# Performance work log

Measured on AMD Instinct MI355X. Metric: run time of the kernel, lower is better.

## Reference

```python
import jax, jax.numpy as jnp
import numpy as np

D_MODEL = 2048
NUM_HEADS = 16
NUM_KV_HEADS = 4
LATENT_DIM = 64
HEAD_DIM = D_MODEL // NUM_HEADS  # 128
GROUP_SIZE = NUM_HEADS // NUM_KV_HEADS  # 4
B, T = 4, 2048


def setup_inputs() -> dict:
    key = jax.random.key(0)
    ks = jax.random.split(key, 9)
    s = lambda fan_in: 1.0 / np.sqrt(fan_in)
    # weights stored as (in, out) so y = x @ W matches torch Linear math
    return {
        "x": jax.random.normal(ks[0], (B, T, D_MODEL), jnp.float32),
        "W_q": jax.random.uniform(ks[1], (D_MODEL, D_MODEL), jnp.float32, -s(D_MODEL), s(D_MODEL)),
        "W_k": jax.random.uniform(ks[2], (D_MODEL, NUM_KV_HEADS * HEAD_DIM), jnp.float32, -s(D_MODEL), s(D_MODEL)),
        "W_v": jax.random.uniform(ks[3], (D_MODEL, NUM_KV_HEADS * HEAD_DIM), jnp.float32, -s(D_MODEL), s(D_MODEL)),
        "W_k_to_latent": jax.random.uniform(ks[4], (HEAD_DIM, LATENT_DIM), jnp.float32, -s(HEAD_DIM), s(HEAD_DIM)),
        "W_v_to_latent": jax.random.uniform(ks[5], (HEAD_DIM, LATENT_DIM), jnp.float32, -s(HEAD_DIM), s(HEAD_DIM)),
        "W_k_from_latent": jax.random.uniform(ks[6], (LATENT_DIM, HEAD_DIM), jnp.float32, -s(LATENT_DIM), s(LATENT_DIM)),
        "W_v_from_latent": jax.random.uniform(ks[7], (LATENT_DIM, HEAD_DIM), jnp.float32, -s(LATENT_DIM), s(LATENT_DIM)),
        "W_o": jax.random.uniform(ks[8], (D_MODEL, D_MODEL), jnp.float32, -s(D_MODEL), s(D_MODEL)),
    }


def reference(x, W_q, W_k, W_v, W_k_to_latent, W_v_to_latent, W_k_from_latent, W_v_from_latent, W_o):
    b, t, _ = x.shape
    # projections
    q = (x @ W_q).reshape(b, t, NUM_HEADS, HEAD_DIM).transpose(0, 2, 1, 3)        # [B,H,T,Dh]
    k = (x @ W_k).reshape(b, t, NUM_KV_HEADS, HEAD_DIM).transpose(0, 2, 1, 3)     # [B,Hkv,T,Dh]
    v = (x @ W_v).reshape(b, t, NUM_KV_HEADS, HEAD_DIM).transpose(0, 2, 1, 3)
    # compress to latent, then restore (explicit, as in the original module)
    k_latent = k @ W_k_to_latent                                                  # [B,Hkv,T,L]
    v_latent = v @ W_v_to_latent
    k_restored = k_latent @ W_k_from_latent                                       # [B,Hkv,T,Dh]
    v_restored = v_latent @ W_v_from_latent
    # GQA tiling: repeat_interleave over head axis
    k_tile = jnp.repeat(k_restored, GROUP_SIZE, axis=1)                           # [B,H,T,Dh]
    v_tile = jnp.repeat(v_restored, GROUP_SIZE, axis=1)
    # explicit attention
    att = jnp.einsum("bhqd,bhkd->bhqk", q, k_tile) / jnp.sqrt(jnp.float32(HEAD_DIM))
    p = jax.nn.softmax(att, axis=-1)
    ctx = jnp.einsum("bhqk,bhkd->bhqd", p, v_tile)                                # [B,H,T,Dh]
    ctx = ctx.transpose(0, 2, 1, 3).reshape(b, t, D_MODEL)
    return ctx @ W_o
```

## Files before the change

### kernel.cpp

```cpp
#include <hip/hip_runtime.h>

typedef __attribute__((ext_vector_type(8))) short short8;
typedef __attribute__((ext_vector_type(4))) float f32x4;
typedef __attribute__((ext_vector_type(16))) float f32x16;
typedef __attribute__((ext_vector_type(4))) unsigned short us4;
typedef __attribute__((ext_vector_type(4))) int i32x4;
typedef __bf16 bf16x2v __attribute__((ext_vector_type(2)));

__device__ __forceinline__ unsigned short f2bf(float f) {
  unsigned u = __builtin_bit_cast(unsigned, f);
  u += 0x7FFFu + ((u >> 16) & 1u);
  return (unsigned short)(u >> 16);
}

__device__ __forceinline__ int packbf(float lo, float hi) {
  bf16x2v v = {(__bf16)lo, (__bf16)hi};
  return __builtin_bit_cast(int, v);
}

__device__ __forceinline__ void gll16(const void* g, void* l) {
  __builtin_amdgcn_global_load_lds(
      (const __attribute__((address_space(1))) void*)g,
      (__attribute__((address_space(3))) void*)l, 16, 0, 0);
}

__device__ __forceinline__ f32x4 MFMA(short8 a, short8 b, f32x4 c) {
  return __builtin_amdgcn_mfma_f32_16x16x32_bf16(a, b, c, 0, 0, 0);
}
__device__ __forceinline__ f32x16 MFMA32(short8 a, short8 b, f32x16 c) {
  return __builtin_amdgcn_mfma_f32_32x32x16_bf16(a, b, c, 0, 0, 0);
}


__global__ void conv_bf16(const float* __restrict__ in, unsigned short* __restrict__ out, int n4) {
  for (int i = blockIdx.x * blockDim.x + threadIdx.x; i < n4; i += gridDim.x * blockDim.x) {
    float4 v = ((const float4*)in)[i];
    us4 o;
    o[0] = f2bf(v.x); o[1] = f2bf(v.y); o[2] = f2bf(v.z); o[3] = f2bf(v.w);
    ((us4*)out)[i] = o;
  }
}

__global__ void t32x2(const float* __restrict__ a, const float* __restrict__ b,
                      float* __restrict__ oa, float* __restrict__ ob) {
  __shared__ float tile[32][33];
  const float* in = blockIdx.z ? b : a;
  float* out = blockIdx.z ? ob : oa;
  int bx = blockIdx.x, by = blockIdx.y;
  int tx = threadIdx.x, ty = threadIdx.y;
#pragma unroll
  for (int i = 0; i < 4; ++i)
    tile[ty + i * 8][tx] = in[(long)(by * 32 + ty + i * 8) * 128 + bx * 32 + tx];
  __syncthreads();
#pragma unroll
  for (int i = 0; i < 4; ++i)
    out[(long)(bx * 32 + ty + i * 8) * 64 + by * 32 + tx] = tile[tx][ty + i * 8];
}

__global__ void fold_q(const float* __restrict__ Wq, const float* __restrict__ WkflT,
                       float* __restrict__ out, float sc) {
  const int t = threadIdx.x;
  const int l = t & 63, wv = t >> 6;
  const int k = blockIdx.x;
  const float* wq = Wq + (long)k * 2048 + wv * 4 * 128;
  float acc[4] = {};
  for (int d = 0; d < 128; ++d) {
    float fv = WkflT[d * 64 + l];
#pragma unroll
    for (int i = 0; i < 4; ++i) acc[i] += wq[i * 128 + d] * fv;
  }
  float* orow = out + (long)k * 1024 + wv * 4 * 64;
#pragma unroll
  for (int i = 0; i < 4; ++i) orow[i * 64 + l] = acc[i] * sc;
}

__global__ void fold_kv2(const float* __restrict__ Wk, const float* __restrict__ Wv,
                         const float* __restrict__ Wk2l, const float* __restrict__ Wv2l,
                         float* __restrict__ out) {
  const int z = blockIdx.z;
  const float* W = z ? Wv : Wk;
  const float* W2l = z ? Wv2l : Wk2l;
  int l = threadIdx.x;
  int k = blockIdx.x;
  int hk = blockIdx.y;
  const float* wr = W + (long)k * 512 + hk * 128;
  float acc = 0.f;
#pragma unroll 8
  for (int d = 0; d < 128; ++d) acc += wr[d] * W2l[d * 64 + l];
  out[(long)k * 512 + z * 256 + hk * 64 + l] = acc;
}

__global__ void tconv2(const float* __restrict__ a, unsigned short* __restrict__ oq,
                       const float* __restrict__ b, unsigned short* __restrict__ okv) {
  __shared__ float tile[32][33];
  int bx = blockIdx.x, by = blockIdx.y;
  int tx = threadIdx.x, ty = threadIdx.y;
  const float* in;
  unsigned short* out;
  int C;
  if (bx < 32) { in = a; out = oq; C = 1024; }
  else         { in = b; out = okv; C = 512; bx -= 32; }
#pragma unroll
  for (int i = 0; i < 4; ++i)
    tile[ty + i * 8][tx] = in[(long)(by * 32 + ty + i * 8) * C + bx * 32 + tx];
  __syncthreads();
#pragma unroll
  for (int i = 0; i < 4; ++i)
    out[(long)(bx * 32 + ty + i * 8) * 2048 + by * 32 + tx] = f2bf(tile[tx][ty + i * 8]);
}

__global__ void fold_o(const float* __restrict__ WvflT, const float* __restrict__ Wo,
                       unsigned short* __restrict__ WoLatT) {
  const int l = threadIdx.x;
  const int j0 = blockIdx.x * 16;
  const int h = blockIdx.y;
  const float* wo = Wo + (long)h * 128 * 2048 + j0;
  float acc[16] = {};
  for (int d = 0; d < 128; ++d) {
    float fv = WvflT[d * 64 + l];
    const float* wr = wo + (long)d * 2048;
#pragma unroll
    for (int jj = 0; jj < 16; ++jj) acc[jj] += fv * wr[jj];
  }
#pragma unroll
  for (int jj = 0; jj < 16; ++jj)
    WoLatT[(long)(j0 + jj) * 1024 + h * 64 + l] = f2bf(acc[jj]);
}

template <int EPI>
__global__ __launch_bounds__(256, 2) void gemm_bt(const unsigned short* __restrict__ A,
                                                  const unsigned short* __restrict__ BT,
                                                  void* __restrict__ Cout, int M, int N, int K) {
  __shared__ unsigned short As[128 * 32];
  __shared__ unsigned short Bs[128 * 32];
  const int tid = threadIdx.x;
  const int lane = tid & 63, w = tid >> 6;
  const int wr = w >> 1, wc = w & 1;
  const int c = lane & 15, hi = lane >> 4;
  const int nbn = N >> 7;
  int bid = blockIdx.x;
  bid = (bid & 7) * (gridDim.x >> 3) + (bid >> 3);
  const int bm = bid / nbn, bn = bid % nbn;
  const int row0 = bm << 7, col0 = bn << 7;

  const unsigned short* ga = A + (long)(row0 + (tid >> 2)) * K + ((tid & 3) << 3);
  const unsigned short* gb = BT + (long)(col0 + (tid >> 2)) * K + ((tid & 3) << 3);
  unsigned short* la = As + tid * 8;
  unsigned short* lb = Bs + tid * 8;
  const long sA = (long)64 * K;

  f32x4 acc[4][4] = {};

  for (int k0 = 0; k0 < K; k0 += 32) {
    __syncthreads();
    gll16(ga + k0, la);
    gll16(ga + sA + k0, la + 2048);
    gll16(gb + k0, lb);
    gll16(gb + sA + k0, lb + 2048);
    __syncthreads();
    short8 a[4], b[4];
#pragma unroll
    for (int m = 0; m < 4; ++m)
      a[m] = *(const short8*)&As[(wr * 64 + m * 16 + c) * 32 + hi * 8];
#pragma unroll
    for (int n = 0; n < 4; ++n)
      b[n] = *(const short8*)&Bs[(wc * 64 + n * 16 + c) * 32 + hi * 8];
#pragma unroll
    for (int m = 0; m < 4; ++m)
#pragma unroll
      for (int n = 0; n < 4; ++n) acc[m][n] = MFMA(a[m], b[n], acc[m][n]);
  }

  if (EPI == 0) {
    unsigned short* C = (unsigned short*)Cout;
#pragma unroll
    for (int m = 0; m < 4; ++m) {
      int r0 = row0 + wr * 64 + m * 16 + hi * 4;
#pragma unroll
      for (int n = 0; n < 4; ++n) {
        int cc = col0 + wc * 64 + n * 16 + c;
#pragma unroll
        for (int j = 0; j < 4; ++j) C[(long)(r0 + j) * N + cc] = f2bf(acc[m][n][j]);
      }
    }
  } else {
    float* C = (float*)Cout;
#pragma unroll
    for (int m = 0; m < 4; ++m) {
      int r0 = row0 + wr * 64 + m * 16 + hi * 4;
#pragma unroll
      for (int n = 0; n < 4; ++n) {
        int cc = col0 + wc * 64 + n * 16 + c;
#pragma unroll
        for (int j = 0; j < 4; ++j) C[(long)(r0 + j) * N + cc] = acc[m][n][j];
      }
    }
  }
}

__global__ __launch_bounds__(256, 2) void gemm_qkv(const unsigned short* __restrict__ A,
                                                   const unsigned short* __restrict__ BT,
                                                   unsigned short* __restrict__ Qout,
                                                   unsigned short* __restrict__ Kout,
                                                   unsigned short* __restrict__ Vout) {
  const int K = 2048;
  __shared__ unsigned short As[128 * 32];
  __shared__ unsigned short Bs[128 * 32];
  const int tid = threadIdx.x;
  const int lane = tid & 63, w = tid >> 6;
  const int wr = w >> 1, wc = w & 1;
  const int c = lane & 15, hi = lane >> 4;
  const int nbn = 12;
  int bid = blockIdx.x;
  bid = (bid & 7) * (gridDim.x >> 3) + (bid >> 3);
  const int bm = bid / nbn, bn = bid % nbn;
  const int row0 = bm << 7, col0 = bn << 7;

  const unsigned short* ga = A + (long)(row0 + (tid >> 2)) * K + ((tid & 3) << 3);
  const unsigned short* gb = BT + (long)(col0 + (tid >> 2)) * K + ((tid & 3) << 3);
  unsigned short* la = As + tid * 8;
  unsigned short* lb = Bs + tid * 8;
  const long sA = (long)64 * K;

  f32x4 acc[4][4] = {};

  for (int k0 = 0; k0 < K; k0 += 32) {
    __syncthreads();
    gll16(ga + k0, la);
    gll16(ga + sA + k0, la + 2048);
    gll16(gb + k0, lb);
    gll16(gb + sA + k0, lb + 2048);
    __syncthreads();
    short8 a[4], b[4];
#pragma unroll
    for (int m = 0; m < 4; ++m)
      a[m] = *(const short8*)&As[(wr * 64 + m * 16 + c) * 32 + hi * 8];
#pragma unroll
    for (int n = 0; n < 4; ++n)
      b[n] = *(const short8*)&Bs[(wc * 64 + n * 16 + c) * 32 + hi * 8];
#pragma unroll
    for (int m = 0; m < 4; ++m)
#pragma unroll
      for (int n = 0; n < 4; ++n) acc[m][n] = MFMA(a[m], b[n], acc[m][n]);
  }

  if (col0 < 1024) {
#pragma unroll
    for (int m = 0; m < 4; ++m) {
      int r0 = row0 + wr * 64 + m * 16 + hi * 4;
#pragma unroll
      for (int n = 0; n < 4; ++n) {
        int cc = col0 + wc * 64 + n * 16 + c;
#pragma unroll
        for (int j = 0; j < 4; ++j) Qout[(long)(r0 + j) * 1024 + cc] = f2bf(acc[m][n][j]);
      }
    }
  } else if (col0 < 1280) {
#pragma unroll
    for (int m = 0; m < 4; ++m) {
      int r0 = row0 + wr * 64 + m * 16 + hi * 4;
#pragma unroll
      for (int n = 0; n < 4; ++n) {
        int cc = col0 - 1024 + wc * 64 + n * 16 + c;
#pragma unroll
        for (int j = 0; j < 4; ++j) Kout[(long)(r0 + j) * 256 + cc] = f2bf(acc[m][n][j]);
      }
    }
  } else {
#pragma unroll
    for (int m = 0; m < 4; ++m) {
      int r0 = row0 + wr * 64 + m * 16 + hi * 4;
#pragma unroll
      for (int n = 0; n < 4; ++n) {
        int cc = col0 - 1280 + wc * 64 + n * 16 + c;
        us4 v;
#pragma unroll
        for (int j = 0; j < 4; ++j) v[j] = f2bf(acc[m][n][j]);
        *(us4*)&Vout[(long)cc * 8192 + r0] = v;
      }
    }
  }
}

__global__ __launch_bounds__(512, 1) void attn_kernel(const unsigned short* __restrict__ Q,
                                                      const unsigned short* __restrict__ Kr,
                                                      const unsigned short* __restrict__ VT,
                                                      unsigned short* __restrict__ CTX) {
  const int qt = blockIdx.x, h = blockIdx.y, b = blockIdx.z;
  const int kvh = h >> 2;
  const int tid = threadIdx.x, lane = tid & 63, w = tid >> 6;
  const int q31 = lane & 31, hi = lane >> 5;

  __shared__ unsigned short Ks[2][64 * 64];
  __shared__ unsigned short Vs[2][64 * 64];

  const long qrow = (long)(b * 2048 + qt * 256 + w * 32 + q31);
  short8 qf[4];
#pragma unroll
  for (int st = 0; st < 4; ++st)
    qf[st] = *(const short8*)&Q[qrow * 1024 + h * 64 + st * 16 + hi * 8];

  f32x16 acc[2] = {};
  f32x16 acc_s = {};
  short8 ones;
#pragma unroll
  for (int e = 0; e < 8; ++e) ones[e] = (short)0x3F80;

  const unsigned short* kbase = Kr + (long)b * 2048 * 256 + kvh * 64;
  const unsigned short* vbase = VT + (long)kvh * 64 * 8192 + b * 2048;

  const int p = tid * 16;
  const int srow = p >> 8;
  const int inb = (p & 255) ^ ((srow & 15) << 4);
  const int skey = srow * 2 + (inb >> 7);
  const long kgo = (long)skey * 256 + ((inb & 127) >> 1);
  const long vgo = (long)skey * 8192 + ((inb & 127) >> 1);

#define STAGE(T, BUF)                                     \
  do {                                                    \
    gll16(kbase + (long)(T) * 16384 + kgo, (char*)Ks[BUF] + p); \
    gll16(vbase + (T) * 64 + vgo, (char*)Vs[BUF] + p);    \
  } while (0)

  STAGE(0, 0);
  __syncthreads();

  const int kr0 = q31 >> 1, kr1 = 16 + (q31 >> 1);
  const int ki0 = (q31 & 1) * 128;
  const int kswz0 = (kr0 & 15) << 4;
  const int kswz1 = (kr1 & 15) << 4;

  for (int t = 0; t < 32; ++t) {
    const int cur = t & 1;
    if (t < 31) STAGE(t + 1, cur ^ 1);

    const char* ks = (const char*)Ks[cur];
    const char* vs = (const char*)Vs[cur];

    f32x16 s0 = {}, s1 = {};
    __builtin_amdgcn_s_setprio(1);
#pragma unroll
    for (int st = 0; st < 4; ++st) {
      int colb = st * 32 + hi * 16;
      short8 k0 = *(const short8*)(ks + kr0 * 256 + ((ki0 + colb) ^ kswz0));
      short8 k1 = *(const short8*)(ks + kr1 * 256 + ((ki0 + colb) ^ kswz1));
      s0 = MFMA32(k0, qf[st], s0);
      s1 = MFMA32(k1, qf[st], s1);
    }
    __builtin_amdgcn_s_setprio(0);

#pragma unroll
    for (int e = 0; e < 16; ++e) s0[e] = __builtin_amdgcn_exp2f(s0[e]);
#pragma unroll
    for (int e = 0; e < 16; ++e) s1[e] = __builtin_amdgcn_exp2f(s1[e]);

    short8 ap[4];
#pragma unroll
    for (int kq = 0; kq < 4; ++kq) {
      int a0, a1, a2, a3;
      if (kq == 0) {
        a0 = packbf(s0[0], s0[1]);   a1 = packbf(s0[2], s0[3]);
        a2 = packbf(s0[4], s0[5]);   a3 = packbf(s0[6], s0[7]);
      } else if (kq == 1) {
        a0 = packbf(s0[8], s0[9]);   a1 = packbf(s0[10], s0[11]);
        a2 = packbf(s0[12], s0[13]); a3 = packbf(s0[14], s0[15]);
      } else if (kq == 2) {
        a0 = packbf(s1[0], s1[1]);   a1 = packbf(s1[2], s1[3]);
        a2 = packbf(s1[4], s1[5]);   a3 = packbf(s1[6], s1[7]);
      } else {
        a0 = packbf(s1[8], s1[9]);   a1 = packbf(s1[10], s1[11]);
        a2 = packbf(s1[12], s1[13]); a3 = packbf(s1[14], s1[15]);
      }
      int off0 = hi ? a0 : a2;
      int off1 = hi ? a1 : a3;
      int r0 = __shfl_xor(off0, 32);
      int r1 = __shfl_xor(off1, 32);
      i32x4 tt;
      tt[0] = hi ? r0 : a0;
      tt[1] = hi ? r1 : a1;
      tt[2] = hi ? a2 : r0;
      tt[3] = hi ? a3 : r1;
      ap[kq] = __builtin_bit_cast(short8, tt);
    }

    __builtin_amdgcn_s_setprio(1);
#pragma unroll
    for (int dblk = 0; dblk < 2; ++dblk) {
      int d = dblk * 32 + q31;
      int vr = d >> 1;
      int vi = (d & 1) * 128;
      int vswz = (vr & 15) << 4;
#pragma unroll
      for (int kq = 0; kq < 4; ++kq) {
        short8 vv = *(const short8*)(vs + vr * 256 + ((vi + kq * 32 + hi * 16) ^ vswz));
        acc[dblk] = MFMA32(ap[kq], vv, acc[dblk]);
      }
    }
#pragma unroll
    for (int kq = 0; kq < 4; ++kq) acc_s = MFMA32(ap[kq], ones, acc_s);
    __builtin_amdgcn_s_setprio(0);

    __syncthreads();
  }

#pragma unroll
  for (int rg = 0; rg < 16; ++rg) {
    int qr = (rg & 3) + 8 * (rg >> 2) + 4 * hi;
    float il = 1.0f / acc_s[rg];
    long grow = (long)(b * 2048 + qt * 256 + w * 32 + qr);
#pragma unroll
    for (int dblk = 0; dblk < 2; ++dblk)
      CTX[grow * 1024 + h * 64 + dblk * 32 + q31] = f2bf(acc[dblk][rg] * il);
  }
#undef STAGE
}


extern "C" void kernel_launch(void* const* d_in, const int* in_sizes, int n_in, void* d_out,
                              int out_size, void* d_ws, size_t ws_size, hipStream_t stream) {
  (void)in_sizes; (void)n_in; (void)out_size; (void)ws_size;
  const float* x    = (const float*)d_in[0];
  const float* W_q  = (const float*)d_in[1];
  const float* W_k  = (const float*)d_in[2];
  const float* W_v  = (const float*)d_in[3];
  const float* Wk2l = (const float*)d_in[4];
  const float* Wv2l = (const float*)d_in[5];
  const float* Wkfl = (const float*)d_in[6];
  const float* Wvfl = (const float*)d_in[7];
  const float* W_o  = (const float*)d_in[8];
  float* out = (float*)d_out;

  char* ws = (char*)d_ws;
  unsigned short* Xb     = (unsigned short*)(ws + 0);
  unsigned short* Qb     = (unsigned short*)(ws + 33554432);
  unsigned short* KRb    = (unsigned short*)(ws + 50331648);
  unsigned short* VTb    = (unsigned short*)(ws + 54525952);
  unsigned short* WqLatT = (unsigned short*)(ws + 58720256);
  unsigned short* WkvT   = (unsigned short*)(ws + 62914560);
  unsigned short* WoLatT = (unsigned short*)(ws + 65011712);
  float* Wstage          = (float*)(ws + 69206016);
  float* Wstage2         = (float*)(ws + 77594624);
  float* WkflT           = (float*)(ws + 81788928);
  float* WvflT           = (float*)(ws + 81821696);
  unsigned short* CTXb = Xb;

  const float sc = (float)(0.088388347648318447 * 1.4426950408889634);

  t32x2<<<dim3(4, 2, 2), dim3(32, 8), 0, stream>>>(Wkfl, Wvfl, WkflT, WvflT);
  conv_bf16<<<2048, 256, 0, stream>>>(x, Xb, 16777216 / 4);
  fold_q<<<2048, 256, 0, stream>>>(W_q, WkflT, Wstage, sc);
  fold_kv2<<<dim3(2048, 4, 2), 64, 0, stream>>>(W_k, W_v, Wk2l, Wv2l, Wstage2);
  tconv2<<<dim3(48, 64), dim3(32, 8), 0, stream>>>(Wstage, WqLatT, Wstage2, WkvT);
  fold_o<<<dim3(128, 16), 64, 0, stream>>>(WvflT, W_o, WoLatT);

  gemm_qkv<<<768, 256, 0, stream>>>(Xb, WqLatT, Qb, KRb, VTb);

  attn_kernel<<<dim3(8, 16, 4), 512, 0, stream>>>(Qb, KRb, VTb, CTXb);

  gemm_bt<2><<<1024, 256, 0, stream>>>(CTXb, WoLatT, out, 8192, 2048, 1024);
}
```

Baseline: 291.4 us.

## Split attention KV range across two blocks and add partial-sum reduce kernel

```diff
diff --git a/kernel.cpp b/kernel.cpp
--- a/kernel.cpp
+++ b/kernel.cpp
@@ -6,6 +6,7 @@
 typedef __attribute__((ext_vector_type(4))) unsigned short us4;
 typedef __attribute__((ext_vector_type(4))) int i32x4;
 typedef __bf16 bf16x2v __attribute__((ext_vector_type(2)));
+typedef _Float16 half4v __attribute__((ext_vector_type(4)));
 
 __device__ __forceinline__ unsigned short f2bf(float f) {
   unsigned u = __builtin_bit_cast(unsigned, f);
@@ -285,14 +286,21 @@
 __global__ __launch_bounds__(512, 1) void attn_kernel(const unsigned short* __restrict__ Q,
                                                       const unsigned short* __restrict__ Kr,
                                                       const unsigned short* __restrict__ VT,
-                                                      unsigned short* __restrict__ CTX) {
-  const int qt = blockIdx.x, h = blockIdx.y, b = blockIdx.z;
+                                                      _Float16* __restrict__ Cp0,
+                                                      _Float16* __restrict__ Cp1,
+                                                      float* __restrict__ Lp0,
+                                                      float* __restrict__ Lp1) {
+  const int qt = blockIdx.x & 7, z = blockIdx.x >> 3;
+  const int h = blockIdx.y, b = blockIdx.z;
   const int kvh = h >> 2;
   const int tid = threadIdx.x, lane = tid & 63, w = tid >> 6;
   const int q31 = lane & 31, hi = lane >> 5;
 
   __shared__ unsigned short Ks[2][64 * 64];
   __shared__ unsigned short Vs[2][64 * 64];
+
+  _Float16* Cp = z ? Cp1 : Cp0;
+  float* Lp = z ? Lp1 : Lp0;
 
   const long qrow = (long)(b * 2048 + qt * 256 + w * 32 + q31);
   short8 qf[4];
@@ -322,7 +330,8 @@
     gll16(vbase + (T) * 64 + vgo, (char*)Vs[BUF] + p);    \
   } while (0)
 
-  STAGE(0, 0);
+  const int t0 = z * 16;
+  STAGE(t0, 0);
   __syncthreads();
 
   const int kr0 = q31 >> 1, kr1 = 16 + (q31 >> 1);
@@ -330,9 +339,9 @@
   const int kswz0 = (kr0 & 15) << 4;
   const int kswz1 = (kr1 & 15) << 4;
 
-  for (int t = 0; t < 32; ++t) {
+  for (int t = 0; t < 16; ++t) {
     const int cur = t & 1;
-    if (t < 31) STAGE(t + 1, cur ^ 1);
+    if (t < 15) STAGE(t0 + t + 1, cur ^ 1);
 
     const char* ks = (const char*)Ks[cur];
     const char* vs = (const char*)Vs[cur];
@@ -406,13 +415,36 @@
 #pragma unroll
   for (int rg = 0; rg < 16; ++rg) {
     int qr = (rg & 3) + 8 * (rg >> 2) + 4 * hi;
-    float il = 1.0f / acc_s[rg];
     long grow = (long)(b * 2048 + qt * 256 + w * 32 + qr);
 #pragma unroll
     for (int dblk = 0; dblk < 2; ++dblk)
-      CTX[grow * 1024 + h * 64 + dblk * 32 + q31] = f2bf(acc[dblk][rg] * il);
+      Cp[grow * 1024 + h * 64 + dblk * 32 + q31] = (_Float16)(acc[dblk][rg] * 0.0625f);
+  }
+  if (q31 == 0) {
+#pragma unroll
+    for (int rg = 0; rg < 16; ++rg) {
+      int qr = (rg & 3) + 8 * (rg >> 2) + 4 * hi;
+      long grow = (long)(b * 2048 + qt * 256 + w * 32 + qr);
+      Lp[grow * 16 + h] = acc_s[rg] * 0.0625f;
+    }
   }
 #undef STAGE
+}
+
+__global__ void attn_reduce(const _Float16* __restrict__ Cp0, const _Float16* __restrict__ Cp1,
+                            const float* __restrict__ Lp0, const float* __restrict__ Lp1,
+                            unsigned short* __restrict__ CTX) {
+  const long row = blockIdx.x;
+  const int t = threadIdx.x;
+  const int col0 = t * 4;
+  const int h = col0 >> 6;
+  const float il = 1.0f / (Lp0[row * 16 + h] + Lp1[row * 16 + h]);
+  half4v c0 = *(const half4v*)(Cp0 + row * 1024 + col0);
+  half4v c1 = *(const half4v*)(Cp1 + row * 1024 + col0);
+  us4 o;
+#pragma unroll
+  for (int j = 0; j < 4; ++j) o[j] = f2bf(((float)c0[j] + (float)c1[j]) * il);
+  *(us4*)&CTX[row * 1024 + col0] = o;
 }
 
 
@@ -442,6 +474,10 @@
   float* Wstage2         = (float*)(ws + 77594624);
   float* WkflT           = (float*)(ws + 81788928);
   float* WvflT           = (float*)(ws + 81821696);
+  _Float16* Cp0          = (_Float16*)(ws + 16777216);
+  _Float16* Cp1          = (_Float16*)(ws + 83886080);
+  float* Lp0             = (float*)(ws + 100663296);
+  float* Lp1             = (float*)(ws + 101187584);
   unsigned short* CTXb = Xb;
 
   const float sc = (float)(0.088388347648318447 * 1.4426950408889634);
@@ -455,7 +491,8 @@
 
   gemm_qkv<<<768, 256, 0, stream>>>(Xb, WqLatT, Qb, KRb, VTb);
 
-  attn_kernel<<<dim3(8, 16, 4), 512, 0, stream>>>(Qb, KRb, VTb, CTXb);
+  attn_kernel<<<dim3(16, 16, 4), 512, 0, stream>>>(Qb, KRb, VTb, Cp0, Cp1, Lp0, Lp1);
+  attn_reduce<<<8192, 256, 0, stream>>>(Cp0, Cp1, Lp0, Lp1, CTXb);
 
   gemm_bt<2><<<1024, 256, 0, stream>>>(CTXb, WoLatT, out, 8192, 2048, 1024);
 }
```

Measured after the change: 325.9 us. 1.12x slower.
